# Kernel optimization log

Hardware: AMD Instinct MI355X
Metric: run time of the kernel (lower is better)

## Reference

```python
import jax, jax.numpy as jnp
import numpy as np

N = 100000      # nodes
E = 1600000     # edges (before self-loops)
T = 35          # temporal length
CT = 16         # temporal conv channels
H = 4           # heads
C = 32          # out channels per head
HC = H * C      # 128
B = 64          # graphs in batch
NEG = 0.2       # leaky relu slope (PyG default)


def _conv1d_relu(x, w, b, stride):
    # x: [N, Cin, L], w: [Cout, Cin, K]
    y = jax.lax.conv_general_dilated(x, w, (stride,), 'VALID',
                                     dimension_numbers=('NCH', 'OIH', 'NCH'))
    return jax.nn.relu(y + b[None, :, None])


def _gatv2(x, src, dst, ea, Wl, Wr, We, att, bias):
    # GATv2Conv (eval mode, add_self_loops=True, fill_value='mean')
    E0 = src.shape[0]
    deg = jax.ops.segment_sum(jnp.ones((E0,), x.dtype), dst, num_segments=N)
    loop_attr = jax.ops.segment_sum(ea, dst, num_segments=N) / jnp.maximum(deg, 1.0)[:, None]
    loops = jnp.arange(N)
    src2 = jnp.concatenate([src, loops])
    dst2 = jnp.concatenate([dst, loops])
    ea2 = jnp.concatenate([ea, loop_attr], axis=0)          # [E+N, 1]
    msg = (x @ Wl)[src2].reshape(-1, H, C)                   # x_j via lin_l
    tgt = (x @ Wr)[dst2].reshape(-1, H, C)                   # x_i via lin_r
    ef = (ea2 @ We).reshape(-1, H, C)                        # lin_edge
    s = jax.nn.leaky_relu(msg + tgt + ef, NEG)
    logits = jnp.einsum('ehc,hc->eh', s, att)                # [E+N, H]
    m = jax.ops.segment_max(logits, dst2, num_segments=N)    # every node has a self-loop
    p = jnp.exp(logits - m[dst2])
    denom = jax.ops.segment_sum(p, dst2, num_segments=N)
    alpha = p / denom[dst2]                                  # segment softmax
    out = jax.ops.segment_sum(msg * alpha[..., None], dst2, num_segments=N)
    return out.reshape(N, HC) + bias


def setup_inputs() -> dict:
    key = jax.random.key(0)
    ks = jax.random.split(key, 20)
    d = {}
    d['x'] = jax.random.normal(ks[0], (N, 1, T), dtype=jnp.float32)
    d['edge_index'] = jax.random.randint(ks[1], (2, E), 0, N)
    d['edge_attr'] = jax.random.normal(ks[2], (E, 1), dtype=jnp.float32)
    d['batch'] = jnp.sort(jax.random.randint(ks[3], (N,), 0, B))
    d['conv1_w'] = jax.random.normal(ks[4], (CT, 1, 3), dtype=jnp.float32) * 0.3
    d['conv1_b'] = jnp.zeros((CT,), jnp.float32)
    d['conv2_w'] = jax.random.normal(ks[5], (CT, CT, 3), dtype=jnp.float32) * 0.15
    d['conv2_b'] = jnp.zeros((CT,), jnp.float32)
    for i, pre in enumerate(['g1', 'g2']):
        kk = jax.random.split(ks[6 + i], 5)
        d[pre + '_Wl'] = jax.random.normal(kk[0], (HC, HC), dtype=jnp.float32) * (1.0 / np.sqrt(HC))
        d[pre + '_Wr'] = jax.random.normal(kk[1], (HC, HC), dtype=jnp.float32) * (1.0 / np.sqrt(HC))
        d[pre + '_We'] = jax.random.normal(kk[2], (1, HC), dtype=jnp.float32)
        d[pre + '_att'] = jax.random.normal(kk[3], (H, C), dtype=jnp.float32) * (1.0 / np.sqrt(C))
        d[pre + '_b'] = jnp.zeros((HC,), jnp.float32)
    d['fc_w'] = jax.random.normal(ks[8], (HC, 1), dtype=jnp.float32) * (1.0 / np.sqrt(HC))
    d['fc_b'] = jnp.zeros((1,), jnp.float32)
    return d


def reference(x, edge_index, edge_attr, batch,
              conv1_w, conv1_b, conv2_w, conv2_b,
              g1_Wl, g1_Wr, g1_We, g1_att, g1_b,
              g2_Wl, g2_Wr, g2_We, g2_att, g2_b,
              fc_w, fc_b):
    h = _conv1d_relu(x, conv1_w, conv1_b, 2)   # [N,16,17]
    h = _conv1d_relu(h, conv2_w, conv2_b, 2)   # [N,16,8]
    h = h.reshape(N, HC)
    src, dst = edge_index[0], edge_index[1]
    h = jax.nn.relu(_gatv2(h, src, dst, edge_attr, g1_Wl, g1_Wr, g1_We, g1_att, g1_b))
    h = jax.nn.relu(_gatv2(h, src, dst, edge_attr, g2_Wl, g2_Wr, g2_We, g2_att, g2_b))
    g = jax.ops.segment_sum(h, batch, num_segments=B)  # global_add_pool
    return (g @ fc_w + fc_b)[:, 0]
```

## Files before the change

kernel.cpp:

```cpp
#include <hip/hip_runtime.h>
#include <hip/hip_fp16.h>
#include <math.h>

#define NN 100000
#define EE 1600000
#define BB 64
#define CAP 48
#define EHALF 800000

#define CONV_B ((NN + 15) / 16)
#define SBH ((EHALF + 2047) / 2048)
#define CONVA_B (CONV_B + SBH)
#define GEMM_B ((NN + 63) / 64)
#define GEMMS_B (GEMM_B + SBH)

typedef _Float16 h2 __attribute__((ext_vector_type(2)));
typedef _Float16 f16x8 __attribute__((ext_vector_type(8)));
typedef float f32x4 __attribute__((ext_vector_type(4)));

__device__ __forceinline__ h2 h2bcast(float v) {
  _Float16 h = (_Float16)v; h2 r = { h, h }; return r;
}

__device__ __forceinline__ h2 lrelu_h2(h2 z) {
  const h2 c = { (_Float16)0.2f, (_Float16)0.2f };
  h2 zz = z * c;
#if __has_builtin(__builtin_elementwise_max)
  return __builtin_elementwise_max(z, zz);
#else
  h2 r; r.x = z.x > zz.x ? z.x : zz.x; r.y = z.y > zz.y ? z.y : zz.y; return r;
#endif
}

__device__ __forceinline__ float fdot2f(h2 a, h2 b, float c) {
#if __has_builtin(__builtin_amdgcn_fdot2)
  return __builtin_amdgcn_fdot2(a, b, c, false);
#else
  return c + (float)a.x * (float)b.x + (float)a.y * (float)b.y;
#endif
}

__device__ __forceinline__ void scatter8(int e0,
    const int* __restrict__ src, const int* __restrict__ dst,
    const float* __restrict__ ea, int* __restrict__ cursor,
    int2* __restrict__ pack)
{
  int4  d0 = *(const int4*)(dst + e0);
  int4  d1 = *(const int4*)(dst + e0 + 4);
  int4  s0 = *(const int4*)(src + e0);
  int4  s1 = *(const int4*)(src + e0 + 4);
  float4 a0 = *(const float4*)(ea + e0);
  float4 a1 = *(const float4*)(ea + e0 + 4);
  int p0 = atomicAdd(cursor + d0.x, 1);
  int p1 = atomicAdd(cursor + d0.y, 1);
  int p2 = atomicAdd(cursor + d0.z, 1);
  int p3 = atomicAdd(cursor + d0.w, 1);
  int p4 = atomicAdd(cursor + d1.x, 1);
  int p5 = atomicAdd(cursor + d1.y, 1);
  int p6 = atomicAdd(cursor + d1.z, 1);
  int p7 = atomicAdd(cursor + d1.w, 1);
  if (p0 < CAP) pack[(size_t)d0.x * CAP + p0] = make_int2(s0.x, __float_as_int(a0.x));
  if (p1 < CAP) pack[(size_t)d0.y * CAP + p1] = make_int2(s0.y, __float_as_int(a0.y));
  if (p2 < CAP) pack[(size_t)d0.z * CAP + p2] = make_int2(s0.z, __float_as_int(a0.z));
  if (p3 < CAP) pack[(size_t)d0.w * CAP + p3] = make_int2(s0.w, __float_as_int(a0.w));
  if (p4 < CAP) pack[(size_t)d1.x * CAP + p4] = make_int2(s1.x, __float_as_int(a1.x));
  if (p5 < CAP) pack[(size_t)d1.y * CAP + p5] = make_int2(s1.y, __float_as_int(a1.y));
  if (p6 < CAP) pack[(size_t)d1.z * CAP + p6] = make_int2(s1.z, __float_as_int(a1.z));
  if (p7 < CAP) pack[(size_t)d1.w * CAP + p7] = make_int2(s1.w, __float_as_int(a1.w));
}

__global__ __launch_bounds__(256) void wpack_kernel(
    const float* __restrict__ Wl0, const float* __restrict__ Wr0,
    const float* __restrict__ Wl1, const float* __restrict__ Wr1,
    unsigned int* __restrict__ Wp)
{
  int t = blockIdx.x * 256 + threadIdx.x;
  int L = t >> 14;
  int rem = t & 16383;
  int ch = rem >> 6;
  int kk = rem & 63;
  const float* W = (L == 0) ? (ch < 128 ? Wl0 : Wr0) : (ch < 128 ? Wl1 : Wr1);
  int c = ch & 127;
  float v0 = W[(2 * kk) * 128 + c];
  float v1 = W[(2 * kk + 1) * 128 + c];
  h2 h = { (_Float16)v0, (_Float16)v1 };
  Wp[t] = __builtin_bit_cast(unsigned int, h);
}

__global__ __launch_bounds__(256) void conv_scatter_kernel(
    const float* __restrict__ x,
    const float* __restrict__ w1, const float* __restrict__ b1,
    const float* __restrict__ w2, const float* __restrict__ b2,
    __half* __restrict__ h16,
    const int* __restrict__ src, const int* __restrict__ dst,
    const float* __restrict__ ea,
    int* __restrict__ cursor, int2* __restrict__ pack)
{
  int tid = threadIdx.x;
  int r17 = blockIdx.x % 17;
  if (r17 == 0) {
    int sid = blockIdx.x / 17;
    int e0 = sid * 2048 + tid * 8;
    if (e0 >= EHALF) return;
    scatter8(e0, src, dst, ea, cursor, pack);
    return;
  }
  int cid = (blockIdx.x / 17) * 16 + (r17 - 1);
  if (cid >= CONV_B) return;
  __shared__ float s_x[16 * 36];
  __shared__ float s_c1[16 * 272];
  int n0 = cid * 16;

  for (int i = tid; i < 16 * 35; i += 256)
    s_x[(i / 35) * 36 + (i % 35)] = x[(size_t)n0 * 35 + i];

  int node = tid >> 4;
  int lane = tid & 15;

  float w1a = w1[lane * 3], w1b = w1[lane * 3 + 1], w1c = w1[lane * 3 + 2];
  float bb1 = b1[lane];
  float bb2 = b2[lane];

  __syncthreads();

  const float* row = s_x + node * 36;
  float xr[36];
#pragma unroll
  for (int i = 0; i < 9; ++i)
    *(float4*)&xr[4 * i] = *(const float4*)&row[4 * i];

  float* c1n = s_c1 + node * 272;
#pragma unroll
  for (int p = 0; p < 17; ++p) {
    float a = fmaf(w1a, xr[2 * p], fmaf(w1b, xr[2 * p + 1], fmaf(w1c, xr[2 * p + 2], bb1)));
    c1n[p * 16 + lane] = fmaxf(a, 0.f);
  }

  float w2r[48];
#pragma unroll
  for (int i = 0; i < 12; ++i)
    *(float4*)&w2r[4 * i] = *(const float4*)&w2[lane * 48 + 4 * i];

  __syncthreads();

  float acc8[8];
#pragma unroll
  for (int t = 0; t < 8; ++t) {
    float acc = bb2;
#pragma unroll
    for (int k = 0; k < 3; ++k) {
      const float4* rp = (const float4*)(c1n + (2 * t + k) * 16);
      float4 r0 = rp[0], r1 = rp[1], r2 = rp[2], r3 = rp[3];
      acc = fmaf(w2r[0  + k], r0.x, acc);
      acc = fmaf(w2r[3  + k], r0.y, acc);
      acc = fmaf(w2r[6  + k], r0.z, acc);
      acc = fmaf(w2r[9  + k], r0.w, acc);
      acc = fmaf(w2r[12 + k], r1.x, acc);
      acc = fmaf(w2r[15 + k], r1.y, acc);
      acc = fmaf(w2r[18 + k], r1.z, acc);
      acc = fmaf(w2r[21 + k], r1.w, acc);
      acc = fmaf(w2r[24 + k], r2.x, acc);
      acc = fmaf(w2r[27 + k], r2.y, acc);
      acc = fmaf(w2r[30 + k], r2.z, acc);
      acc = fmaf(w2r[33 + k], r2.w, acc);
      acc = fmaf(w2r[36 + k], r3.x, acc);
      acc = fmaf(w2r[39 + k], r3.y, acc);
      acc = fmaf(w2r[42 + k], r3.z, acc);
      acc = fmaf(w2r[45 + k], r3.w, acc);
    }
    acc8[t] = fmaxf(acc, 0.f);
  }

  h2 q0 = { (_Float16)acc8[0], (_Float16)acc8[1] };
  h2 q1 = { (_Float16)acc8[2], (_Float16)acc8[3] };
  h2 q2 = { (_Float16)acc8[4], (_Float16)acc8[5] };
  h2 q3 = { (_Float16)acc8[6], (_Float16)acc8[7] };
  int4 pk;
  pk.x = __builtin_bit_cast(int, q0);
  pk.y = __builtin_bit_cast(int, q1);
  pk.z = __builtin_bit_cast(int, q2);
  pk.w = __builtin_bit_cast(int, q3);
  *(int4*)(h16 + (size_t)(n0 + node) * 128 + lane * 8) = pk;
}

__global__ __launch_bounds__(256) void gemm_dual(
    const __half* __restrict__ A16, const unsigned int* __restrict__ WpT,
    __half* __restrict__ Cl, __half* __restrict__ Cr,
    const int* __restrict__ src, const int* __restrict__ dst,
    const float* __restrict__ ea,
    int* __restrict__ cursor, int2* __restrict__ pack, int with_scatter)
{
  int tid = threadIdx.x;
  int gid = blockIdx.x;
  if (with_scatter) {
    int r5 = blockIdx.x % 5;
    if (r5 == 0) {
      int sid = blockIdx.x / 5;
      int e0 = EHALF + sid * 2048 + tid * 8;
      if (e0 >= EE) return;
      scatter8(e0, src, dst, ea, cursor, pack);
      return;
    }
    gid = (blockIdx.x / 5) * 4 + (r5 - 1);
    if (gid >= GEMM_B) return;
  }

  __shared__ uint4 sB[64 * 16];
  int row0 = gid * 64;
  for (int u = tid; u < 64 * 16; u += 256) {
    int node = u >> 4, cu = u & 15;
    uint4 v = { 0u, 0u, 0u, 0u };
    if (row0 + node < NN)
      v = *(const uint4*)(A16 + (size_t)(row0 + node) * 128 + cu * 8);
    sB[node * 16 + (cu ^ (node & 7))] = v;
  }
  __syncthreads();

  int wv = tid >> 6;
  int l  = tid & 63;
  int lr = l & 15;
  int lq = l >> 4;

  f32x4 acc[4][4];
#pragma unroll
  for (int ct = 0; ct < 4; ++ct)
#pragma unroll
    for (int nt = 0; nt < 4; ++nt)
      acc[ct][nt] = (f32x4){ 0.f, 0.f, 0.f, 0.f };

#pragma unroll
  for (int kc = 0; kc < 4; ++kc) {
    f16x8 afrag[4];
#pragma unroll
    for (int ct = 0; ct < 4; ++ct) {
      int ch = wv * 64 + ct * 16 + lr;
      int4 w = *(const int4*)(WpT + ch * 64 + kc * 16 + lq * 4);
      afrag[ct] = __builtin_bit_cast(f16x8, w);
    }
    f16x8 bfrag[4];
#pragma unroll
    for (int nt = 0; nt < 4; ++nt) {
      int node = nt * 16 + lr;
      int unit = kc * 4 + lq;
      uint4 v = sB[node * 16 + (unit ^ (node & 7))];
      bfrag[nt] = __builtin_bit_cast(f16x8, v);
    }
#pragma unroll
    for (int ct = 0; ct < 4; ++ct)
#pragma unroll
      for (int nt = 0; nt < 4; ++nt)
        acc[ct][nt] = __builtin_amdgcn_mfma_f32_16x16x32_f16(
            afrag[ct], bfrag[nt], acc[ct][nt], 0, 0, 0);
  }

  __half* Cb = (wv < 2) ? Cl : Cr;
#pragma unroll
  for (int ct = 0; ct < 4; ++ct) {
    int chm = ((wv & 1) * 64) + ct * 16 + lq * 4;
#pragma unroll
    for (int nt = 0; nt < 4; ++nt) {
      int node = row0 + nt * 16 + lr;
      if (node < NN) {
        h2 v0 = { (_Float16)acc[ct][nt][0], (_Float16)acc[ct][nt][1] };
        h2 v1 = { (_Float16)acc[ct][nt][2], (_Float16)acc[ct][nt][3] };
        uint2 u;
        u.x = __builtin_bit_cast(unsigned int, v0);
        u.y = __builtin_bit_cast(unsigned int, v1);
        *(uint2*)(Cb + (size_t)node * 128 + chm) = u;
      }
    }
  }
}

__device__ __forceinline__ float edge_logit16(const h2 m0, const h2 m1, const h2 m2, const h2 m3,
                                              h2 wh, const h2* hrd, const h2* we, const h2* at)
{
  h2 z0 = m0 + (hrd[0] + wh * we[0]);
  h2 z1 = m1 + (hrd[1] + wh * we[1]);
  h2 z2 = m2 + (hrd[2] + wh * we[2]);
  h2 z3 = m3 + (hrd[3] + wh * we[3]);
  h2 s0 = lrelu_h2(z0);
  h2 s1 = lrelu_h2(z1);
  h2 s2 = lrelu_h2(z2);
  h2 s3 = lrelu_h2(z3);
  float pf;
  pf = fdot2f(s0, at[0], 0.f);
  pf = fdot2f(s1, at[1], pf);
  pf = fdot2f(s2, at[2], pf);
  pf = fdot2f(s3, at[3], pf);
  pf += __shfl_xor(pf, 1, 4);
  pf += __shfl_xor(pf, 2, 4);
  return pf;
}

#define LOADM(dst, idx) { int4 raw_ = *(const int4*)(hl + (size_t)(idx) * 128 + j8); \
  dst##0 = __builtin_bit_cast(h2, raw_.x); dst##1 = __builtin_bit_cast(h2, raw_.y);  \
  dst##2 = __builtin_bit_cast(h2, raw_.z); dst##3 = __builtin_bit_cast(h2, raw_.w); }

__global__ __launch_bounds__(256) void gat_node_kernel(
    const int* __restrict__ cnt_arr, const int2* __restrict__ pack,
    const __half* __restrict__ hl, const __half* __restrict__ hr,
    const float* __restrict__ We, const float* __restrict__ att,
    const float* __restrict__ bias, __half* __restrict__ out)
{
  int n = blockIdx.x * 16 + (threadIdx.x >> 4);
  if (n >= NN) return;
  int lq = threadIdx.x & 15;
  int j8 = lq * 8;

  const float RLN2 = 1.44269504088896340736f;
  int4 hraw = *(const int4*)(hr + (size_t)n * 128 + j8);
  h2 hrd[4] = { __builtin_bit_cast(h2, hraw.x), __builtin_bit_cast(h2, hraw.y),
                __builtin_bit_cast(h2, hraw.z), __builtin_bit_cast(h2, hraw.w) };
  float4 wf0 = *(const float4*)(We + j8);
  float4 wf1 = *(const float4*)(We + j8 + 4);
  h2 we[4] = { { (_Float16)wf0.x, (_Float16)wf0.y }, { (_Float16)wf0.z, (_Float16)wf0.w },
               { (_Float16)wf1.x, (_Float16)wf1.y }, { (_Float16)wf1.z, (_Float16)wf1.w } };
  float4 af0 = *(const float4*)(att + j8);
  float4 af1 = *(const float4*)(att + j8 + 4);
  h2 at[4] = { { (_Float16)(af0.x * RLN2), (_Float16)(af0.y * RLN2) },
               { (_Float16)(af0.z * RLN2), (_Float16)(af0.w * RLN2) },
               { (_Float16)(af1.x * RLN2), (_Float16)(af1.y * RLN2) },
               { (_Float16)(af1.z * RLN2), (_Float16)(af1.w * RLN2) } };

  int cnt = cnt_arr[n]; if (cnt > CAP) cnt = CAP;
  const int2* p = pack + (size_t)n * CAP;

  float m = -INFINITY, l = 0.f, wsum = 0.f;
  h2 zh = { (_Float16)0.f, (_Float16)0.f };
  h2 acc0 = zh, acc1 = zh, acc2 = zh, acc3 = zh;

  int nb = cnt >> 2;
  int4 ca = { 0, 0, 0, 0 }, cb = { 0, 0, 0, 0 };
  h2 nr10, nr11, nr12, nr13, nr20, nr21, nr22, nr23;
  h2 nr30, nr31, nr32, nr33, nr40, nr41, nr42, nr43;
  if (nb > 0) {
    const int4* p4 = (const int4*)p;
    ca = p4[0]; cb = p4[1];
    LOADM(nr1, ca.x); LOADM(nr2, ca.z); LOADM(nr3, cb.x); LOADM(nr4, cb.z);
  }
  for (int b = 0; b < nb; ++b) {
    int4 da = ca, db = cb;
    h2 m10 = nr10, m11 = nr11, m12 = nr12, m13 = nr13;
    h2 m20 = nr20, m21 = nr21, m22 = nr22, m23 = nr23;
    h2 m30 = nr30, m31 = nr31, m32 = nr32, m33 = nr33;
    h2 m40 = nr40, m41 = nr41, m42 = nr42, m43 = nr43;
    if (b + 1 < nb) {
      const int4* p4 = (const int4*)(p + (b + 1) * 4);
      ca = p4[0]; cb = p4[1];
      LOADM(nr1, ca.x); LOADM(nr2, ca.z); LOADM(nr3, cb.x); LOADM(nr4, cb.z);
    }
    float w1 = __int_as_float(da.y), w2 = __int_as_float(da.w);
    float w3 = __int_as_float(db.y), w4 = __int_as_float(db.w);
    wsum += (w1 + w2) + (w3 + w4);
    float p1 = edge_logit16(m10, m11, m12, m13, h2bcast(w1), hrd, we, at);
    float p2 = edge_logit16(m20, m21, m22, m23, h2bcast(w2), hrd, we, at);
    float p3 = edge_logit16(m30, m31, m32, m33, h2bcast(w3), hrd, we, at);
    float p4v = edge_logit16(m40, m41, m42, m43, h2bcast(w4), hrd, we, at);
    float mn = fmaxf(fmaxf(m, fmaxf(p1, p2)), fmaxf(p3, p4v));
    float sc = exp2f(m - mn);
    float t1 = exp2f(p1 - mn);
    float t2 = exp2f(p2 - mn);
    float t3 = exp2f(p3 - mn);
    float t4 = exp2f(p4v - mn);
    l = fmaf(l, sc, (t1 + t2) + (t3 + t4));
    h2 sch = h2bcast(sc);
    h2 t1h = h2bcast(t1), t2h = h2bcast(t2), t3h = h2bcast(t3), t4h = h2bcast(t4);
    acc0 = acc0 * sch + (t1h * m10 + (t2h * m20 + (t3h * m30 + t4h * m40)));
    acc1 = acc1 * sch + (t1h * m11 + (t2h * m21 + (t3h * m31 + t4h * m41)));
    acc2 = acc2 * sch + (t1h * m12 + (t2h * m22 + (t3h * m32 + t4h * m42)));
    acc3 = acc3 * sch + (t1h * m13 + (t2h * m23 + (t3h * m33 + t4h * m43)));
    m = mn;
  }
  for (int i = nb * 4; i < cnt; ++i) {
    int2 v1 = p[i];
    float w1 = __int_as_float(v1.y);
    h2 mm0, mm1, mm2, mm3;
    LOADM(mm, v1.x);
    wsum += w1;
    float p1 = edge_logit16(mm0, mm1, mm2, mm3, h2bcast(w1), hrd, we, at);
    float mn = fmaxf(m, p1);
    float sc = exp2f(m - mn);
    float t1 = exp2f(p1 - mn);
    l = fmaf(l, sc, t1);
    h2 sch = h2bcast(sc), t1h = h2bcast(t1);
    acc0 = acc0 * sch + t1h * mm0;
    acc1 = acc1 * sch + t1h * mm1;
    acc2 = acc2 * sch + t1h * mm2;
    acc3 = acc3 * sch + t1h * mm3;
    m = mn;
  }

  float la = wsum / fmaxf((float)cnt, 1.f);
  h2 sl0, sl1, sl2, sl3;
  LOADM(sl, n);
  float ps = edge_logit16(sl0, sl1, sl2, sl3, h2bcast(la), hrd, we, at);
  float mn = fmaxf(m, ps);
  float sc = exp2f(m - mn);
  float ts = exp2f(ps - mn);
  l = fmaf(l, sc, ts);
  h2 sch = h2bcast(sc), tsh = h2bcast(ts);
  acc0 = acc0 * sch + tsh * sl0;
  acc1 = acc1 * sch + tsh * sl1;
  acc2 = acc2 * sch + tsh * sl2;
  acc3 = acc3 * sch + tsh * sl3;

  float inv = 1.f / l;
  float4 b0 = *(const float4*)(bias + j8);
  float4 b1 = *(const float4*)(bias + j8 + 4);
  h2 o0 = { (_Float16)fmaxf(fmaf((float)acc0.x, inv, b0.x), 0.f),
            (_Float16)fmaxf(fmaf((float)acc0.y, inv, b0.y), 0.f) };
  h2 o1 = { (_Float16)fmaxf(fmaf((float)acc1.x, inv, b0.z), 0.f),
            (_Float16)fmaxf(fmaf((float)acc1.y, inv, b0.w), 0.f) };
  h2 o2 = { (_Float16)fmaxf(fmaf((float)acc2.x, inv, b1.x), 0.f),
            (_Float16)fmaxf(fmaf((float)acc2.y, inv, b1.y), 0.f) };
  h2 o3 = { (_Float16)fmaxf(fmaf((float)acc3.x, inv, b1.z), 0.f),
            (_Float16)fmaxf(fmaf((float)acc3.y, inv, b1.w), 0.f) };
  int4 pk;
  pk.x = __builtin_bit_cast(int, o0);
  pk.y = __builtin_bit_cast(int, o1);
  pk.z = __builtin_bit_cast(int, o2);
  pk.w = __builtin_bit_cast(int, o3);
  *(int4*)(out + (size_t)n * 128 + j8) = pk;
}

__global__ __launch_bounds__(128) void pool_kernel(
    const __half* __restrict__ h, const int* __restrict__ batch,
    float* __restrict__ pooled)
{
  int n0 = blockIdx.x * 64;
  if (n0 >= NN) return;
  int j = threadIdx.x;
  int nend = n0 + 64; if (nend > NN) nend = NN;
  float acc = 0.f;
  int curb = batch[n0];
  for (int n = n0; n < nend; ++n) {
    int b = batch[n];
    if (b != curb) {
      unsafeAtomicAdd(pooled + curb * 128 + j, acc);
      acc = 0.f; curb = b;
    }
    acc += __half2float(h[(size_t)n * 128 + j]);
  }
  unsafeAtomicAdd(pooled + curb * 128 + j, acc);
}

__global__ __launch_bounds__(128) void fc_kernel(
    const float* __restrict__ pooled, const float* __restrict__ fcw,
    const float* __restrict__ fcb, float* __restrict__ out)
{
  int b = blockIdx.x;
  int t = threadIdx.x;
  float v = pooled[b * 128 + t] * fcw[t];
#pragma unroll
  for (int off = 32; off >= 1; off >>= 1) v += __shfl_down(v, off, 64);
  __shared__ float sbuf[2];
  if ((t & 63) == 0) sbuf[t >> 6] = v;
  __syncthreads();
  if (t == 0) out[b] = sbuf[0] + sbuf[1] + fcb[0];
}

extern "C" void kernel_launch(void* const* d_in, const int* in_sizes, int n_in,
                              void* d_out, int out_size, void* d_ws, size_t ws_size,
                              hipStream_t stream)
{
  const float* x    = (const float*)d_in[0];
  const int*   ei   = (const int*)d_in[1];
  const float* ea   = (const float*)d_in[2];
  const int*   batch= (const int*)d_in[3];
  const float* c1w  = (const float*)d_in[4];
  const float* c1b  = (const float*)d_in[5];
  const float* c2w  = (const float*)d_in[6];
  const float* c2b  = (const float*)d_in[7];
  const float* gWl[2] = { (const float*)d_in[8],  (const float*)d_in[13] };
  const float* gWr[2] = { (const float*)d_in[9],  (const float*)d_in[14] };
  const float* gWe[2] = { (const float*)d_in[10], (const float*)d_in[15] };
  const float* gAt[2] = { (const float*)d_in[11], (const float*)d_in[16] };
  const float* gB [2] = { (const float*)d_in[12], (const float*)d_in[17] };
  const float* fcw  = (const float*)d_in[18];
  const float* fcb  = (const float*)d_in[19];
  float* out = (float*)d_out;

  const int* src = ei;
  const int* dst = ei + EE;

  __half* h16    = (__half*)d_ws;
  __half* hl     = h16 + (size_t)NN * 128;
  __half* hr     = hl + (size_t)NN * 128;
  int2*  pack    = (int2*)(hr + (size_t)NN * 128);
  int*   cursor  = (int*)(pack + (size_t)NN * CAP);
  float* pooled  = (float*)(cursor + NN);
  unsigned int* Wp = (unsigned int*)(pooled + BB * 128);

  hipMemsetAsync(cursor, 0, NN * sizeof(int), stream);
  hipMemsetAsync(pooled, 0, BB * 128 * sizeof(float), stream);

  wpack_kernel<<<128, 256, 0, stream>>>(gWl[0], gWr[0], gWl[1], gWr[1], Wp);

  conv_scatter_kernel<<<CONVA_B, 256, 0, stream>>>(
      x, c1w, c1b, c2w, c2b, h16, src, dst, ea, cursor, pack);

  for (int L = 0; L < 2; ++L) {
    gemm_dual<<<(L == 0 ? GEMMS_B : GEMM_B), 256, 0, stream>>>(
        h16, Wp + L * 16384, hl, hr, src, dst, ea, cursor, pack, L == 0 ? 1 : 0);
    gat_node_kernel<<<(NN + 15) / 16, 256, 0, stream>>>(cursor, pack, hl, hr,
                                                        gWe[L], gAt[L], gB[L], h16);
  }

  pool_kernel<<<(NN + 63) / 64, 128, 0, stream>>>(h16, batch, pooled);
  fc_kernel<<<BB, 128, 0, stream>>>(pooled, fcw, fcb, out);
}
```

Before: 419.8 us.

## Sort nodes by in-degree bucket for GAT load balance and fold cursor memset

Adds a counting sort (histogram, prefix, placement kernels) that orders nodes by clamped in-degree, so each GAT node block processes nodes of similar edge counts and wavefront divergence drops. The cursor memset is folded into the weight-pack kernel, and the attention dot product now accumulates in packed fp16 before a single float conversion. This costs three small extra launches plus an indirection read, and the fp16 accumulation lowers logit precision. Output writes through the order array become scattered rather than contiguous.

After: 422.8 us. About the same (+0.7%).

```diff
diff --git a/kernel.cpp b/kernel.cpp
--- a/kernel.cpp
+++ b/kernel.cpp
@@ -13,6 +13,7 @@
 #define CONVA_B (CONV_B + SBH)
 #define GEMM_B ((NN + 63) / 64)
 #define GEMMS_B (GEMM_B + SBH)
+#define NODE_B ((NN + 255) / 256)
 
 typedef _Float16 h2 __attribute__((ext_vector_type(2)));
 typedef _Float16 f16x8 __attribute__((ext_vector_type(8)));
@@ -29,14 +30,6 @@
   return __builtin_elementwise_max(z, zz);
 #else
   h2 r; r.x = z.x > zz.x ? z.x : zz.x; r.y = z.y > zz.y ? z.y : zz.y; return r;
-#endif
-}
-
-__device__ __forceinline__ float fdot2f(h2 a, h2 b, float c) {
-#if __has_builtin(__builtin_amdgcn_fdot2)
-  return __builtin_amdgcn_fdot2(a, b, c, false);
-#else
-  return c + (float)a.x * (float)b.x + (float)a.y * (float)b.y;
 #endif
 }
 
@@ -72,19 +65,79 @@
 __global__ __launch_bounds__(256) void wpack_kernel(
     const float* __restrict__ Wl0, const float* __restrict__ Wr0,
     const float* __restrict__ Wl1, const float* __restrict__ Wr1,
-    unsigned int* __restrict__ Wp)
+    unsigned int* __restrict__ Wp, int* __restrict__ cursor,
+    int* __restrict__ gcnt)
 {
   int t = blockIdx.x * 256 + threadIdx.x;
-  int L = t >> 14;
-  int rem = t & 16383;
-  int ch = rem >> 6;
-  int kk = rem & 63;
-  const float* W = (L == 0) ? (ch < 128 ? Wl0 : Wr0) : (ch < 128 ? Wl1 : Wr1);
-  int c = ch & 127;
-  float v0 = W[(2 * kk) * 128 + c];
-  float v1 = W[(2 * kk + 1) * 128 + c];
-  h2 h = { (_Float16)v0, (_Float16)v1 };
-  Wp[t] = __builtin_bit_cast(unsigned int, h);
+  if (t < NN) cursor[t] = 0;
+  if (t < CAP + 1) gcnt[t] = 0;
+  if (t < 32768) {
+    int L = t >> 14;
+    int rem = t & 16383;
+    int ch = rem >> 6;
+    int kk = rem & 63;
+    const float* W = (L == 0) ? (ch < 128 ? Wl0 : Wr0) : (ch < 128 ? Wl1 : Wr1);
+    int c = ch & 127;
+    float v0 = W[(2 * kk) * 128 + c];
+    float v1 = W[(2 * kk + 1) * 128 + c];
+    h2 h = { (_Float16)v0, (_Float16)v1 };
+    Wp[t] = __builtin_bit_cast(unsigned int, h);
+  }
+}
+
+__global__ __launch_bounds__(256) void hist_kernel(
+    const int* __restrict__ cursor, int* __restrict__ gcnt)
+{
+  __shared__ int hh[CAP + 1];
+  int tid = threadIdx.x;
+  if (tid <= CAP) hh[tid] = 0;
+  __syncthreads();
+  int n = blockIdx.x * 256 + tid;
+  int c = -1;
+  if (n < NN) {
+    c = cursor[n]; if (c > CAP) c = CAP;
+    atomicAdd(&hh[c], 1);
+  }
+  __syncthreads();
+  if (tid <= CAP && hh[tid] > 0) atomicAdd(&gcnt[tid], hh[tid]);
+}
+
+__global__ __launch_bounds__(64) void prefix_kernel(
+    const int* __restrict__ gcnt, int* __restrict__ gbase)
+{
+  if (threadIdx.x == 0) {
+    int s = 0;
+    for (int i = 0; i <= CAP; ++i) { gbase[i] = s; s += gcnt[i]; }
+  }
+}
+
+__global__ __launch_bounds__(256) void place_kernel(
+    const int* __restrict__ cursor, int* __restrict__ gbase,
+    int* __restrict__ order)
+{
+  __shared__ int lh[CAP + 1];
+  __shared__ int lb[CAP + 1];
+  int tid = threadIdx.x;
+  if (tid <= CAP) lh[tid] = 0;
+  __syncthreads();
+  int n = blockIdx.x * 256 + tid;
+  int c = 0;
+  if (n < NN) {
+    c = cursor[n]; if (c > CAP) c = CAP;
+    atomicAdd(&lh[c], 1);
+  }
+  __syncthreads();
+  if (tid <= CAP) {
+    int cnt = lh[tid];
+    lb[tid] = cnt > 0 ? atomicAdd(&gbase[tid], cnt) : 0;
+  }
+  __syncthreads();
+  if (tid <= CAP) lh[tid] = 0;
+  __syncthreads();
+  if (n < NN) {
+    int s = atomicAdd(&lh[c], 1);
+    order[lb[c] + s] = n;
+  }
 }
 
 __global__ __launch_bounds__(256) void conv_scatter_kernel(
@@ -279,15 +332,11 @@
   h2 z1 = m1 + (hrd[1] + wh * we[1]);
   h2 z2 = m2 + (hrd[2] + wh * we[2]);
   h2 z3 = m3 + (hrd[3] + wh * we[3]);
-  h2 s0 = lrelu_h2(z0);
-  h2 s1 = lrelu_h2(z1);
-  h2 s2 = lrelu_h2(z2);
-  h2 s3 = lrelu_h2(z3);
-  float pf;
-  pf = fdot2f(s0, at[0], 0.f);
-  pf = fdot2f(s1, at[1], pf);
-  pf = fdot2f(s2, at[2], pf);
-  pf = fdot2f(s3, at[3], pf);
+  h2 d = lrelu_h2(z0) * at[0];
+  d = lrelu_h2(z1) * at[1] + d;
+  d = lrelu_h2(z2) * at[2] + d;
+  d = lrelu_h2(z3) * at[3] + d;
+  float pf = (float)d.x + (float)d.y;
   pf += __shfl_xor(pf, 1, 4);
   pf += __shfl_xor(pf, 2, 4);
   return pf;
@@ -298,13 +347,15 @@
   dst##2 = __builtin_bit_cast(h2, raw_.z); dst##3 = __builtin_bit_cast(h2, raw_.w); }
 
 __global__ __launch_bounds__(256) void gat_node_kernel(
+    const int* __restrict__ order,
     const int* __restrict__ cnt_arr, const int2* __restrict__ pack,
     const __half* __restrict__ hl, const __half* __restrict__ hr,
     const float* __restrict__ We, const float* __restrict__ att,
     const float* __restrict__ bias, __half* __restrict__ out)
 {
-  int n = blockIdx.x * 16 + (threadIdx.x >> 4);
-  if (n >= NN) return;
+  int idx = blockIdx.x * 16 + (threadIdx.x >> 4);
+  if (idx >= NN) return;
+  int n = order[idx];
   int lq = threadIdx.x & 15;
   int j8 = lq * 8;
 
@@ -491,21 +542,32 @@
   int*   cursor  = (int*)(pack + (size_t)NN * CAP);
   float* pooled  = (float*)(cursor + NN);
   unsigned int* Wp = (unsigned int*)(pooled + BB * 128);
-
-  hipMemsetAsync(cursor, 0, NN * sizeof(int), stream);
+  int*   order   = (int*)(Wp + 32768);
+  int*   gcnt    = order + NN;
+  int*   gbase   = gcnt + (CAP + 1);
+
   hipMemsetAsync(pooled, 0, BB * 128 * sizeof(float), stream);
 
-  wpack_kernel<<<128, 256, 0, stream>>>(gWl[0], gWr[0], gWl[1], gWr[1], Wp);
+  wpack_kernel<<<NODE_B, 256, 0, stream>>>(gWl[0], gWr[0], gWl[1], gWr[1],
+                                           Wp, cursor, gcnt);
 
   conv_scatter_kernel<<<CONVA_B, 256, 0, stream>>>(
       x, c1w, c1b, c2w, c2b, h16, src, dst, ea, cursor, pack);
 
-  for (int L = 0; L < 2; ++L) {
-    gemm_dual<<<(L == 0 ? GEMMS_B : GEMM_B), 256, 0, stream>>>(
-        h16, Wp + L * 16384, hl, hr, src, dst, ea, cursor, pack, L == 0 ? 1 : 0);
-    gat_node_kernel<<<(NN + 15) / 16, 256, 0, stream>>>(cursor, pack, hl, hr,
-                                                        gWe[L], gAt[L], gB[L], h16);
-  }
+  gemm_dual<<<GEMMS_B, 256, 0, stream>>>(
+      h16, Wp, hl, hr, src, dst, ea, cursor, pack, 1);
+
+  hist_kernel<<<NODE_B, 256, 0, stream>>>(cursor, gcnt);
+  prefix_kernel<<<1, 64, 0, stream>>>(gcnt, gbase);
+  place_kernel<<<NODE_B, 256, 0, stream>>>(cursor, gbase, order);
+
+  gat_node_kernel<<<(NN + 15) / 16, 256, 0, stream>>>(order, cursor, pack, hl, hr,
+                                                      gWe[0], gAt[0], gB[0], h16);
+
+  gemm_dual<<<GEMM_B, 256, 0, stream>>>(
+      h16, Wp + 16384, hl, hr, src, dst, ea, cursor, pack, 0);
+  gat_node_kernel<<<(NN + 15) / 16, 256, 0, stream>>>(order, cursor, pack, hl, hr,
+                                                      gWe[1], gAt[1], gB[1], h16);
 
   pool_kernel<<<(NN + 63) / 64, 128, 0, stream>>>(h16, batch, pooled);
   fc_kernel<<<BB, 128, 0, stream>>>(pooled, fcw, fcb, out);
```
